# Kernel optimization log

Measured on AMD Instinct MI355X. Metric: run time of the kernel, lower is better.

## Reference

```python
import jax, jax.numpy as jnp
import numpy as np

TEMPERATURE = 0.5
NEG_FILL = -1e9


def setup_inputs() -> dict:
    key = jax.random.key(0)
    k1, k2 = jax.random.split(key)
    B, D = 4096, 256
    z1 = jax.random.normal(k1, (B, D), dtype=jnp.float32)
    z2 = jax.random.normal(k2, (B, D), dtype=jnp.float32)
    return {"z1": z1, "z2": z2}


def reference(z1, z2):
    z = jnp.concatenate([z1, z2], axis=0)           # [n, d], n = 2B
    n = z.shape[0]
    half = n // 2
    sim = jnp.matmul(z, z.T) / TEMPERATURE          # [n, n]
    eye = jnp.eye(n, dtype=bool)
    sim = jnp.where(eye, NEG_FILL, sim)
    # targets: positive pair is the other view of the same sample
    idx = jnp.arange(n)
    targets = jnp.where(idx < half, idx + half, idx - half)
    logp = jax.nn.log_softmax(sim, axis=-1)         # stable softmax CE
    loss = -jnp.mean(jnp.take_along_axis(logp, targets[:, None], axis=1))
    return loss
```

## Files before the change

kernel.cpp:

```cpp
#include <hip/hip_runtime.h>

#define NROWS 8192
#define HALF  4096
#define DIM   256
#define JS    16
#define JRANGE 512
#define JTILES 32
#define IPB   128
#define IPW   32

typedef short bf16x8 __attribute__((ext_vector_type(8)));
typedef float f32x4  __attribute__((ext_vector_type(4)));

#define GLOAD16(g, l) __builtin_amdgcn_global_load_lds( \
    (const __attribute__((address_space(1))) unsigned int*)(g), \
    (__attribute__((address_space(3))) unsigned int*)(l), 16, 0, 0)

__device__ __forceinline__ unsigned short f2bf(float f) {
    unsigned int u = __float_as_uint(f);
    u += 0x7FFFu + ((u >> 16) & 1u);
    return (unsigned short)(u >> 16);
}

__global__ void k_prep(const float* __restrict__ z1, const float* __restrict__ z2,
                       unsigned short* __restrict__ zb, float* __restrict__ pos,
                       float* __restrict__ out) {
    if (blockIdx.x == 0 && threadIdx.x == 0) *out = 0.0f;
    const float R2 = 1.41421356237309515f;
    int w = threadIdx.x >> 6, lane = threadIdx.x & 63;
    int row = blockIdx.x * 4 + w;
    float4 a = *(const float4*)(z1 + (size_t)row * DIM + lane * 4);
    float4 b = *(const float4*)(z2 + (size_t)row * DIM + lane * 4);

    uint2 pa, pb;
    pa.x = (unsigned int)f2bf(a.x*R2) | ((unsigned int)f2bf(a.y*R2) << 16);
    pa.y = (unsigned int)f2bf(a.z*R2) | ((unsigned int)f2bf(a.w*R2) << 16);
    pb.x = (unsigned int)f2bf(b.x*R2) | ((unsigned int)f2bf(b.y*R2) << 16);
    pb.y = (unsigned int)f2bf(b.z*R2) | ((unsigned int)f2bf(b.w*R2) << 16);
    *(uint2*)(zb + (size_t)row * DIM + lane * 4)          = pa;
    *(uint2*)(zb + (size_t)(row + HALF) * DIM + lane * 4) = pb;

    float d = a.x * b.x + a.y * b.y + a.z * b.z + a.w * b.w;
    #pragma unroll
    for (int k = 32; k; k >>= 1) d += __shfl_xor(d, k);
    if (lane == 0) pos[row] = 2.0f * d;
}

__global__ __launch_bounds__(256, 4)
void k_main(const unsigned short* __restrict__ zb, float2* __restrict__ part) {
    __shared__ __align__(16) char lds[4][8192];
    char* ldsflat = &lds[0][0];

    const int tid  = threadIdx.x;
    const int w    = tid >> 6;
    const int lane = tid & 63;
    const int col  = lane & 15;
    const int kg   = lane >> 4;
    const int ib   = blockIdx.x & 63;
    const int js   = blockIdx.x >> 6;
    const int iw   = ib * IPB + w * IPW;
    const int jb0  = js * JRANGE;
    const int swz  = (lane & 7) << 4;
    const int dr   = col - kg * 4;

    const char* zbb = (const char*)zb;

    const int jp0 = w * 1024 + lane * 16;
    const int jp1 = 4096 + jp0;
    const int jg0 = jp0 ^ (((jp0 >> 9) & 7) << 4);
    const int jg1 = jp1 ^ (((jp1 >> 9) & 7) << 4);

    bf16x8 bf[2][8];
    {
        int igo[4];
        #pragma unroll
        for (int k = 0; k < 4; ++k) {
            int p = k * 4096 + w * 1024 + lane * 16;
            igo[k] = p ^ (((p >> 9) & 7) << 4);
        }
        #pragma unroll
        for (int q = 0; q < 4; ++q) {
            const char* gib = zbb + (size_t)(ib * IPB + q * 32) * 512;
            #pragma unroll
            for (int k = 0; k < 4; ++k)
                GLOAD16(gib + igo[k], ldsflat + k * 4096 + w * 1024);
            __syncthreads();
            if (q == w) {
                #pragma unroll
                for (int h = 0; h < 2; ++h) {
                    const char* tb = ldsflat + h * 8192;
                    #pragma unroll
                    for (int kk = 0; kk < 8; ++kk)
                        bf[h][kk] =
                            *(const bf16x8*)(tb + col * 512 + (((kk << 6) | (kg << 4)) ^ swz));
                }
            }
            __syncthreads();
        }
    }

    float m[2], l[2];
    m[0] = m[1] = -1e30f;
    l[0] = l[1] = 0.0f;

    const char* ap = ldsflat + col * 512;
    int aoff[8];
    #pragma unroll
    for (int kk = 0; kk < 8; ++kk) aoff[kk] = ((kk << 6) | (kg << 4)) ^ swz;

    const int dt = (iw - jb0) >> 4;
    const char* jbase = zbb + (size_t)jb0 * 512;

#define JSTAGE(T, B) do { \
    GLOAD16(jbase + (size_t)(T) * 8192 + jg0, ldsflat + (B) * 8192 + w * 1024); \
    GLOAD16(jbase + (size_t)(T) * 8192 + jg1, ldsflat + (B) * 8192 + 4096 + w * 1024); \
} while (0)

#define MASKD(X) do { \
    _Pragma("unroll") \
    for (int r = 0; r < 4; ++r) if (dr == r) X[r] = -1e30f; \
} while (0)

#define LSE_UPD(X, is_) do { \
    float t0 = fmaxf(fmaxf(X[0], X[1]), fmaxf(X[2], X[3])); \
    if (__any(t0 > m[is_])) { \
        float mn = fmaxf(m[is_], t0); \
        l[is_] *= __expf(m[is_] - mn); \
        m[is_] = mn; \
    } \
    l[is_] += __expf(X[0] - m[is_]) + __expf(X[1] - m[is_]) \
            + __expf(X[2] - m[is_]) + __expf(X[3] - m[is_]); \
} while (0)

#define COMPUTE_TILE(B, T) do { \
    f32x4 a0 = {0.f, 0.f, 0.f, 0.f}; \
    f32x4 a1 = a0; \
    bf16x8 af[4]; \
    _Pragma("unroll") \
    for (int kk = 0; kk < 4; ++kk) \
        af[kk] = *(const bf16x8*)(ap + aoff[kk] + (B) * 8192); \
    _Pragma("unroll") \
    for (int kk = 0; kk < 4; ++kk) { \
        a0 = __builtin_amdgcn_mfma_f32_16x16x32_bf16(af[kk], bf[0][kk], a0, 0, 0, 0); \
        a1 = __builtin_amdgcn_mfma_f32_16x16x32_bf16(af[kk], bf[1][kk], a1, 0, 0, 0); \
    } \
    _Pragma("unroll") \
    for (int kk = 0; kk < 4; ++kk) \
        af[kk] = *(const bf16x8*)(ap + aoff[kk + 4] + (B) * 8192); \
    _Pragma("unroll") \
    for (int kk = 0; kk < 4; ++kk) { \
        a0 = __builtin_amdgcn_mfma_f32_16x16x32_bf16(af[kk], bf[0][kk + 4], a0, 0, 0, 0); \
        a1 = __builtin_amdgcn_mfma_f32_16x16x32_bf16(af[kk], bf[1][kk + 4], a1, 0, 0, 0); \
    } \
    const int dd = (T) - dt; \
    if (dd == 0) MASKD(a0); \
    if (dd == 1) MASKD(a1); \
    LSE_UPD(a0, 0); \
    LSE_UPD(a1, 1); \
} while (0)

    JSTAGE(0, 0); JSTAGE(1, 1);
    __syncthreads();

    for (int u = 0; u < 8; ++u) {
        const int t = u * 4;
        JSTAGE(t + 2, 2); JSTAGE(t + 3, 3);
        COMPUTE_TILE(0, t);
        COMPUTE_TILE(1, t + 1);
        __syncthreads();
        if (u < 7) { JSTAGE(t + 4, 0); JSTAGE(t + 5, 1); }
        COMPUTE_TILE(2, t + 2);
        COMPUTE_TILE(3, t + 3);
        __syncthreads();
    }

    #pragma unroll
    for (int is = 0; is < 2; ++is) {
        float mm = m[is], ll = l[is];
        #pragma unroll
        for (int msk = 16; msk <= 32; msk <<= 1) {
            float mo  = __shfl_xor(mm, msk);
            float lo_ = __shfl_xor(ll, msk);
            float mn  = fmaxf(mm, mo);
            ll = ll * __expf(mm - mn) + lo_ * __expf(mo - mn);
            mm = mn;
        }
        if (kg == 0) {
            int i = iw + is * 16 + col;
            part[i * JS + js] = make_float2(mm, ll);
        }
    }
#undef JSTAGE
#undef MASKD
#undef LSE_UPD
#undef COMPUTE_TILE
}

__global__ void k_final(const float2* __restrict__ part, const float* __restrict__ pos,
                        float* __restrict__ out) {
    int tid = threadIdx.x;
    int i = blockIdx.x * 256 + tid;
    const float2* p = part + (size_t)i * JS;
    float2 v[JS];
    float M = -3e30f;
    #pragma unroll
    for (int s = 0; s < JS; ++s) { v[s] = p[s]; M = fmaxf(M, v[s].x); }
    float L = 0.0f;
    #pragma unroll
    for (int s = 0; s < JS; ++s) L += v[s].y * __expf(v[s].x - M);
    float loss = M + __logf(L) - pos[i & (HALF - 1)];

    #pragma unroll
    for (int k = 32; k; k >>= 1) loss += __shfl_down(loss, k);
    __shared__ float ps[4];
    int w = tid >> 6, lane = tid & 63;
    if (lane == 0) ps[w] = loss;
    __syncthreads();
    if (tid == 0) atomicAdd(out, (ps[0] + ps[1] + ps[2] + ps[3]) * (1.0f / (float)NROWS));
}

extern "C" void kernel_launch(void* const* d_in, const int* in_sizes, int n_in,
                              void* d_out, int out_size, void* d_ws, size_t ws_size,
                              hipStream_t stream) {
    const float* z1 = (const float*)d_in[0];
    const float* z2 = (const float*)d_in[1];
    float* out = (float*)d_out;

    char* ws = (char*)d_ws;
    unsigned short* zb = (unsigned short*)ws;
    float* pos  = (float*)(ws + 4u * 1024u * 1024u);
    float2* part = (float2*)(ws + 4u * 1024u * 1024u + 65536u);

    k_prep <<<1024, 256, 0, stream>>>(z1, z2, zb, pos, out);
    k_main <<<1024, 256, 0, stream>>>(zb, part);
    k_final<<<32,   256, 0, stream>>>(part, pos, out);
}
```

Measured before the change: 100.6 us.

## Drop LDS staging; load j-tiles directly from global into registers

Removes the shared-memory staging path (global_load_lds plus barriers) and has each wave load its j-tile fragments straight from global memory into registers, double-buffered across two register sets. The j range per block is halved and the grid doubled to 2048 blocks, giving 32 partials per row, and launch bounds drop to 3 waves per SIMD to fit the larger register footprint. The aim is to remove LDS traffic and synchronisation, at the cost of redundant global/L2 reads across the four waves of a block and more registers per thread.

```diff
diff --git a/kernel.cpp b/kernel.cpp
--- a/kernel.cpp
+++ b/kernel.cpp
@@ -3,18 +3,14 @@
 #define NROWS 8192
 #define HALF  4096
 #define DIM   256
-#define JS    16
-#define JRANGE 512
-#define JTILES 32
+#define JS    32
+#define JRANGE 256
+#define JTILES 16
 #define IPB   128
 #define IPW   32
 
 typedef short bf16x8 __attribute__((ext_vector_type(8)));
 typedef float f32x4  __attribute__((ext_vector_type(4)));
-
-#define GLOAD16(g, l) __builtin_amdgcn_global_load_lds( \
-    (const __attribute__((address_space(1))) unsigned int*)(g), \
-    (__attribute__((address_space(3))) unsigned int*)(l), 16, 0, 0)
 
 __device__ __forceinline__ unsigned short f2bf(float f) {
     unsigned int u = __float_as_uint(f);
@@ -46,11 +42,8 @@
     if (lane == 0) pos[row] = 2.0f * d;
 }
 
-__global__ __launch_bounds__(256, 4)
+__global__ __launch_bounds__(256, 3)
 void k_main(const unsigned short* __restrict__ zb, float2* __restrict__ part) {
-    __shared__ __align__(16) char lds[4][8192];
-    char* ldsflat = &lds[0][0];
-
     const int tid  = threadIdx.x;
     const int w    = tid >> 6;
     const int lane = tid & 63;
@@ -60,60 +53,28 @@
     const int js   = blockIdx.x >> 6;
     const int iw   = ib * IPB + w * IPW;
     const int jb0  = js * JRANGE;
-    const int swz  = (lane & 7) << 4;
     const int dr   = col - kg * 4;
+    const int dt   = (iw - jb0) >> 4;
 
     const char* zbb = (const char*)zb;
-
-    const int jp0 = w * 1024 + lane * 16;
-    const int jp1 = 4096 + jp0;
-    const int jg0 = jp0 ^ (((jp0 >> 9) & 7) << 4);
-    const int jg1 = jp1 ^ (((jp1 >> 9) & 7) << 4);
 
     bf16x8 bf[2][8];
     {
-        int igo[4];
-        #pragma unroll
-        for (int k = 0; k < 4; ++k) {
-            int p = k * 4096 + w * 1024 + lane * 16;
-            igo[k] = p ^ (((p >> 9) & 7) << 4);
-        }
-        #pragma unroll
-        for (int q = 0; q < 4; ++q) {
-            const char* gib = zbb + (size_t)(ib * IPB + q * 32) * 512;
-            #pragma unroll
-            for (int k = 0; k < 4; ++k)
-                GLOAD16(gib + igo[k], ldsflat + k * 4096 + w * 1024);
-            __syncthreads();
-            if (q == w) {
-                #pragma unroll
-                for (int h = 0; h < 2; ++h) {
-                    const char* tb = ldsflat + h * 8192;
-                    #pragma unroll
-                    for (int kk = 0; kk < 8; ++kk)
-                        bf[h][kk] =
-                            *(const bf16x8*)(tb + col * 512 + (((kk << 6) | (kg << 4)) ^ swz));
-                }
-            }
-            __syncthreads();
-        }
-    }
-
-    float m[2], l[2];
-    m[0] = m[1] = -1e30f;
-    l[0] = l[1] = 0.0f;
-
-    const char* ap = ldsflat + col * 512;
-    int aoff[8];
-    #pragma unroll
-    for (int kk = 0; kk < 8; ++kk) aoff[kk] = ((kk << 6) | (kg << 4)) ^ swz;
-
-    const int dt = (iw - jb0) >> 4;
-    const char* jbase = zbb + (size_t)jb0 * 512;
-
-#define JSTAGE(T, B) do { \
-    GLOAD16(jbase + (size_t)(T) * 8192 + jg0, ldsflat + (B) * 8192 + w * 1024); \
-    GLOAD16(jbase + (size_t)(T) * 8192 + jg1, ldsflat + (B) * 8192 + 4096 + w * 1024); \
+        const char* bp = zbb + ((size_t)(iw + col) << 9) + kg * 16;
+        #pragma unroll
+        for (int kk = 0; kk < 8; ++kk) bf[0][kk] = *(const bf16x8*)(bp + kk * 64);
+        #pragma unroll
+        for (int kk = 0; kk < 8; ++kk) bf[1][kk] = *(const bf16x8*)(bp + 8192 + kk * 64);
+    }
+
+    float m0 = -1e30f, m1 = -1e30f, l0 = 0.0f, l1 = 0.0f;
+
+    const char* pa = zbb + ((size_t)(jb0 + col) << 9) + kg * 16;
+
+#define LOADAF(AF, OFF) do { \
+    _Pragma("unroll") \
+    for (int kk = 0; kk < 8; ++kk) \
+        AF[kk] = *(const bf16x8*)(pa + (OFF) + kk * 64); \
 } while (0)
 
 #define MASKD(X) do { \
@@ -121,62 +82,65 @@
     for (int r = 0; r < 4; ++r) if (dr == r) X[r] = -1e30f; \
 } while (0)
 
-#define LSE_UPD(X, is_) do { \
+#define LSE0(X) do { \
     float t0 = fmaxf(fmaxf(X[0], X[1]), fmaxf(X[2], X[3])); \
-    if (__any(t0 > m[is_])) { \
-        float mn = fmaxf(m[is_], t0); \
-        l[is_] *= __expf(m[is_] - mn); \
-        m[is_] = mn; \
+    if (__any(t0 > m0)) { \
+        float mn = fmaxf(m0, t0); \
+        l0 *= __expf(m0 - mn); \
+        m0 = mn; \
     } \
-    l[is_] += __expf(X[0] - m[is_]) + __expf(X[1] - m[is_]) \
-            + __expf(X[2] - m[is_]) + __expf(X[3] - m[is_]); \
-} while (0)
-
-#define COMPUTE_TILE(B, T) do { \
+    l0 += __expf(X[0] - m0) + __expf(X[1] - m0) \
+        + __expf(X[2] - m0) + __expf(X[3] - m0); \
+} while (0)
+
+#define LSE1(X) do { \
+    float t0 = fmaxf(fmaxf(X[0], X[1]), fmaxf(X[2], X[3])); \
+    if (__any(t0 > m1)) { \
+        float mn = fmaxf(m1, t0); \
+        l1 *= __expf(m1 - mn); \
+        m1 = mn; \
+    } \
+    l1 += __expf(X[0] - m1) + __expf(X[1] - m1) \
+        + __expf(X[2] - m1) + __expf(X[3] - m1); \
+} while (0)
+
+#define COMP(AF, T) do { \
     f32x4 a0 = {0.f, 0.f, 0.f, 0.f}; \
     f32x4 a1 = a0; \
-    bf16x8 af[4]; \
     _Pragma("unroll") \
-    for (int kk = 0; kk < 4; ++kk) \
-        af[kk] = *(const bf16x8*)(ap + aoff[kk] + (B) * 8192); \
-    _Pragma("unroll") \
-    for (int kk = 0; kk < 4; ++kk) { \
-        a0 = __builtin_amdgcn_mfma_f32_16x16x32_bf16(af[kk], bf[0][kk], a0, 0, 0, 0); \
-        a1 = __builtin_amdgcn_mfma_f32_16x16x32_bf16(af[kk], bf[1][kk], a1, 0, 0, 0); \
-    } \
-    _Pragma("unroll") \
-    for (int kk = 0; kk < 4; ++kk) \
-        af[kk] = *(const bf16x8*)(ap + aoff[kk + 4] + (B) * 8192); \
-    _Pragma("unroll") \
-    for (int kk = 0; kk < 4; ++kk) { \
-        a0 = __builtin_amdgcn_mfma_f32_16x16x32_bf16(af[kk], bf[0][kk + 4], a0, 0, 0, 0); \
-        a1 = __builtin_amdgcn_mfma_f32_16x16x32_bf16(af[kk], bf[1][kk + 4], a1, 0, 0, 0); \
+    for (int kk = 0; kk < 8; ++kk) { \
+        a0 = __builtin_amdgcn_mfma_f32_16x16x32_bf16(AF[kk], bf[0][kk], a0, 0, 0, 0); \
+        a1 = __builtin_amdgcn_mfma_f32_16x16x32_bf16(AF[kk], bf[1][kk], a1, 0, 0, 0); \
     } \
     const int dd = (T) - dt; \
     if (dd == 0) MASKD(a0); \
     if (dd == 1) MASKD(a1); \
-    LSE_UPD(a0, 0); \
-    LSE_UPD(a1, 1); \
-} while (0)
-
-    JSTAGE(0, 0); JSTAGE(1, 1);
-    __syncthreads();
-
-    for (int u = 0; u < 8; ++u) {
-        const int t = u * 4;
-        JSTAGE(t + 2, 2); JSTAGE(t + 3, 3);
-        COMPUTE_TILE(0, t);
-        COMPUTE_TILE(1, t + 1);
-        __syncthreads();
-        if (u < 7) { JSTAGE(t + 4, 0); JSTAGE(t + 5, 1); }
-        COMPUTE_TILE(2, t + 2);
-        COMPUTE_TILE(3, t + 3);
-        __syncthreads();
-    }
-
-    #pragma unroll
-    for (int is = 0; is < 2; ++is) {
-        float mm = m[is], ll = l[is];
+    LSE0(a0); \
+    LSE1(a1); \
+} while (0)
+
+    bf16x8 af0[8], af1[8];
+    LOADAF(af0, 0);
+    #pragma unroll
+    for (int u = 0; u < JTILES / 2 - 1; ++u) {
+        LOADAF(af1, 8192);
+        COMP(af0, 2 * u);
+        LOADAF(af0, 16384);
+        COMP(af1, 2 * u + 1);
+        pa += 16384;
+    }
+    LOADAF(af1, 8192);
+    COMP(af0, JTILES - 2);
+    COMP(af1, JTILES - 1);
+
+#undef LOADAF
+#undef MASKD
+#undef LSE0
+#undef LSE1
+#undef COMP
+
+    {
+        float mm = m0, ll = l0;
         #pragma unroll
         for (int msk = 16; msk <= 32; msk <<= 1) {
             float mo  = __shfl_xor(mm, msk);
@@ -185,15 +149,20 @@
             ll = ll * __expf(mm - mn) + lo_ * __expf(mo - mn);
             mm = mn;
         }
-        if (kg == 0) {
-            int i = iw + is * 16 + col;
-            part[i * JS + js] = make_float2(mm, ll);
+        if (kg == 0) part[(size_t)(iw + col) * JS + js] = make_float2(mm, ll);
+    }
+    {
+        float mm = m1, ll = l1;
+        #pragma unroll
+        for (int msk = 16; msk <= 32; msk <<= 1) {
+            float mo  = __shfl_xor(mm, msk);
+            float lo_ = __shfl_xor(ll, msk);
+            float mn  = fmaxf(mm, mo);
+            ll = ll * __expf(mm - mn) + lo_ * __expf(mo - mn);
+            mm = mn;
         }
-    }
-#undef JSTAGE
-#undef MASKD
-#undef LSE_UPD
-#undef COMPUTE_TILE
+        if (kg == 0) part[(size_t)(iw + 16 + col) * JS + js] = make_float2(mm, ll);
+    }
 }
 
 __global__ void k_final(const float2* __restrict__ part, const float* __restrict__ pos,
@@ -230,8 +199,8 @@
     unsigned short* zb = (unsigned short*)ws;
     float* pos  = (float*)(ws + 4u * 1024u * 1024u);
     float2* part = (float2*)(ws + 4u * 1024u * 1024u + 65536u);
-
+    
     k_prep <<<1024, 256, 0, stream>>>(z1, z2, zb, pos, out);
-    k_main <<<1024, 256, 0, stream>>>(zb, part);
+    k_main <<<2048, 256, 0, stream>>>(zb, part);
     k_final<<<32,   256, 0, stream>>>(part, pos, out);
 }
```

Result: slower. 256.8 us (+155.3%).
